# Performance work log

Hardware: AMD Instinct MI355X
Metric: run time of the kernel (lower is better)

Reference implementation:

```python
import jax, jax.numpy as jnp
import numpy as np

B, D_IN, FD = 32768, 2048, 128
N1 = N2 = N3 = 4
T = 1.0  # temperature buffer value (eval mode)
LN_EPS = 1e-5

def _gelu(x):
    return jax.nn.gelu(x, approximate=False)  # torch nn.GELU default = exact erf

def setup_inputs() -> dict:
    key = jax.random.key(0)
    ks = iter(jax.random.split(key, 64))
    def rn(shape, s=0.02):
        return jax.random.normal(next(ks), shape, jnp.float32) * s
    inp = {"x": jax.random.normal(next(ks), (B, D_IN), jnp.float32)}
    # input_proj: Linear(2048,512) GELU Linear(512,256) LayerNorm(256)
    inp.update(ipW1=rn((D_IN, 512)), ipb1=jnp.zeros(512), ipW2=rn((512, 256)), ipb2=jnp.zeros(256),
               ln_g=jnp.ones(256), ln_b=jnp.zeros(256))
    def level(din, nc, pfx):
        return {pfx+"W3d": rn((din, 3)), pfx+"b3d": jnp.zeros(3),
                pfx+"c": rn((nc, 3), 0.3), pfx+"lr": jnp.zeros(nc),
                pfx+"f1W": rn((din, FD)), pfx+"f1b": jnp.zeros(FD),
                pfx+"f2W": rn((FD, FD)), pfx+"f2b": jnp.zeros(FD),
                pfx+"rW": rn((FD+3, nc)), pfx+"rb": jnp.zeros(nc)}
    inp.update(level(256, N1, "l1"))
    inp.update(level(FD, N2, "l2"))
    inp.update(level(FD, N3, "l3"))
    # expert_head: Linear(128+4+4+4, 256) GELU Linear(256, 64)
    inp.update(ehW1=rn((FD+N1+N2+N3, 256)), ehb1=jnp.zeros(256),
               ehW2=rn((256, N1*N2*N3)), ehb2=jnp.zeros(N1*N2*N3))
    return inp

def _level_fwd(x, W3d, b3d, c, f1W, f1b, f2W, f2b, rW, rb):
    # x: (B, din) -> probs (B, nc), features (B, FD)
    pos = x @ W3d + b3d                                   # (B, 3)
    d_sq = ((pos[:, None, :] - c[None, :, :]) ** 2).sum(-1)  # (B, nc)
    geo = -d_sq / (2.0 * T * T + 1e-8)                    # non-spectral geo signal
    feat = _gelu(x @ f1W + f1b) @ f2W + f2b               # (B, FD)
    logits = jnp.concatenate([feat, pos], axis=-1) @ rW + rb + 0.5 * geo
    probs = jax.nn.softmax(logits / max(T, 0.1), axis=-1)  # eval path: plain softmax
    return probs, feat

def _router_fwd(x, ipW1, ipb1, ipW2, ipb2, ln_g, ln_b,
                l1W3d, l1b3d, l1c, l1f1W, l1f1b, l1f2W, l1f2b, l1rW, l1rb,
                l2W3d, l2b3d, l2c, l2f1W, l2f1b, l2f2W, l2f2b, l2rW, l2rb,
                l3W3d, l3b3d, l3c, l3f1W, l3f1b, l3f2W, l3f2b, l3rW, l3rb,
                ehW1, ehb1, ehW2, ehb2):
    h = _gelu(x @ ipW1 + ipb1) @ ipW2 + ipb2
    mu = h.mean(-1, keepdims=True)
    var = ((h - mu) ** 2).mean(-1, keepdims=True)
    h = (h - mu) * jax.lax.rsqrt(var + LN_EPS) * ln_g + ln_b  # LayerNorm(256)
    p1, f1 = _level_fwd(h,  l1W3d, l1b3d, l1c, l1f1W, l1f1b, l1f2W, l1f2b, l1rW, l1rb)
    p2, f2 = _level_fwd(f1, l2W3d, l2b3d, l2c, l2f1W, l2f1b, l2f2W, l2f2b, l2rW, l2rb)
    p3, f3 = _level_fwd(f2, l3W3d, l3b3d, l3c, l3f1W, l3f1b, l3f2W, l3f2b, l3rW, l3rb)
    combined = jnp.concatenate([f3, p1, p2, p3], axis=-1)  # (B, 140)
    logits = _gelu(combined @ ehW1 + ehb1) @ ehW2 + ehb2   # (B, 64)
    expert_probs = jax.nn.softmax(logits / max(T, 0.1), axis=-1)
    return expert_probs

def reference(x, ipW1, ipb1, ipW2, ipb2, ln_g, ln_b,
              l1W3d, l1b3d, l1c, l1lr, l1f1W, l1f1b, l1f2W, l1f2b, l1rW, l1rb,
              l2W3d, l2b3d, l2c, l2lr, l2f1W, l2f1b, l2f2W, l2f2b, l2rW, l2rb,
              l3W3d, l3b3d, l3c, l3lr, l3f1W, l3f1b, l3f2W, l3f2b, l3rW, l3rb,
              ehW1, ehb1, ehW2, ehb2):
    # l?lr (log_radii) are unused in non-spectral mode, matching the source.
    expert_probs = _router_fwd(x, ipW1, ipb1, ipW2, ipb2, ln_g, ln_b,
                               l1W3d, l1b3d, l1c, l1f1W, l1f1b, l1f2W, l1f2b, l1rW, l1rb,
                               l2W3d, l2b3d, l2c, l2f1W, l2f1b, l2f2W, l2f2b, l2rW, l2rb,
                               l3W3d, l3b3d, l3c, l3f1W, l3f1b, l3f2W, l3f2b, l3rW, l3rb,
                               ehW1, ehb1, ehW2, ehb2)
    expert_ids = jnp.argmax(expert_probs, axis=-1)
    return expert_probs, expert_ids
```

## Files before the change

kernel.cpp:

```cpp
#include <hip/hip_runtime.h>
#include <hip/hip_bf16.h>
#include <cstdint>
#include <cstddef>


typedef short  s8v  __attribute__((ext_vector_type(8)));
typedef float  f4v  __attribute__((ext_vector_type(4)));
typedef float  f16v __attribute__((ext_vector_type(16)));
typedef unsigned int u32;

#define B_ROWS 32768

__device__ inline short f2bf(float x) {
    __hip_bfloat16 h = __float2bfloat16(x);
    return __builtin_bit_cast(short, h);
}
__device__ inline float bf2f(short s) {
    return __bfloat162float(__builtin_bit_cast(__hip_bfloat16, s));
}
__device__ inline float gelu_f(float x) {
    return 0.5f * x * (1.0f + erff(x * 0.70710678118654752440f));
}
__device__ inline void gload_lds16(const short* g, short* l) {
    __builtin_amdgcn_global_load_lds(
        (const __attribute__((address_space(1))) u32*)g,
        (__attribute__((address_space(3))) u32*)l, 16, 0, 0);
}

__global__ void split_w1_img(const float* __restrict__ W, short* __restrict__ img)
{
    const int idx = blockIdx.x * 256 + threadIdx.x;
    const int p = idx & 7;
    const int n = (idx >> 3) & 511;
    const int t = idx >> 12;
    const int cs = p ^ (n & 7);
    const int plane = cs >> 2, kc = cs & 3;
    const int kbase = t * 32 + kc * 8;
    s8v v8;
    #pragma unroll
    for (int e = 0; e < 8; ++e) {
        const float v = W[(size_t)(kbase + e) * 512 + n];
        const short h = f2bf(v);
        v8[e] = plane ? f2bf(v - bf2f(h)) : h;
    }
    *(s8v*)&img[(size_t)((t * 512 + n) * 64 + p * 8)] = v8;
}

__launch_bounds__(256, 4)
__global__ void gemm1k(const float* __restrict__ X,
                       const short* __restrict__ Bimg,
                       const float* __restrict__ bias,
                       float* __restrict__ out)
{
    __shared__ short smem[128 * 64 * 2];
    short* Ab = smem;
    short* Bb = smem + 128 * 64;

    const int tid = threadIdx.x;
    const int l = tid & 63, wid = tid >> 6;
    const int wr = wid >> 1, wc = wid & 1;

    const int d = blockIdx.x;
    const int xcd = d & 7, s = d >> 3;
    const int m0 = (xcd * 32 + (s >> 2)) * 128;
    const int n0 = (s & 3) * 128;

    const int ar = tid & 127, ah = tid >> 7;
    const float* xP = X + (size_t)(m0 + ar) * 2048 + ah * 16;
    short* awr = Ab + ar * 64;
    const int pw0 = ((ah * 2    ) ^ (ar & 7)) * 8;
    const int pw1 = ((ah * 2 + 1) ^ (ar & 7)) * 8;
    const int pw2 = ((ah * 2 + 4) ^ (ar & 7)) * 8;
    const int pw3 = ((ah * 2 + 5) ^ (ar & 7)) * 8;

    const short* bP = Bimg + (size_t)n0 * 64 + (size_t)(wid * 4) * 512 + (size_t)l * 8;
    short* bD = Bb + wid * 4 * 512;

    f16v acc[2][2];
    #pragma unroll
    for (int m = 0; m < 2; ++m)
        #pragma unroll
        for (int n = 0; n < 2; ++n) acc[m][n] = (f16v)0.0f;

    f4v cur0, cur1, cur2, cur3;
    cur0 = *(const f4v*)(xP + 0);
    cur1 = *(const f4v*)(xP + 4);
    cur2 = *(const f4v*)(xP + 8);
    cur3 = *(const f4v*)(xP + 12);

    for (int t = 0; t < 64; ++t) {
        s8v hi0, hi1, lo0, lo1;
        #pragma unroll
        for (int e = 0; e < 4; ++e) {
            float v;
            short h;
            v = cur0[e]; h = f2bf(v); hi0[e]     = h; lo0[e]     = f2bf(v - bf2f(h));
            v = cur1[e]; h = f2bf(v); hi0[e + 4] = h; lo0[e + 4] = f2bf(v - bf2f(h));
            v = cur2[e]; h = f2bf(v); hi1[e]     = h; lo1[e]     = f2bf(v - bf2f(h));
            v = cur3[e]; h = f2bf(v); hi1[e + 4] = h; lo1[e + 4] = f2bf(v - bf2f(h));
        }
        __syncthreads();
        *(s8v*)&awr[pw0] = hi0;
        *(s8v*)&awr[pw1] = hi1;
        *(s8v*)&awr[pw2] = lo0;
        *(s8v*)&awr[pw3] = lo1;
        {
            const short* bt = bP + (size_t)t * 32768;
            gload_lds16(bt,          bD);
            gload_lds16(bt +  512,   bD + 512);
            gload_lds16(bt + 1024,   bD + 1024);
            gload_lds16(bt + 1536,   bD + 1536);
        }
        if (t < 63) {
            const float* p = xP + (t + 1) * 32;
            cur0 = *(const f4v*)(p + 0);
            cur1 = *(const f4v*)(p + 4);
            cur2 = *(const f4v*)(p + 8);
            cur3 = *(const f4v*)(p + 12);
        }
        __syncthreads();

        #pragma unroll
        for (int ks = 0; ks < 2; ++ks) {
            const int ph0 = ks * 2 + (l >> 5);
            s8v ahf[2], alf[2], bhf[2], blf[2];
            #pragma unroll
            for (int m = 0; m < 2; ++m) {
                const int row = wr * 64 + m * 32 + (l & 31);
                const int ph = ph0 ^ (row & 7);
                ahf[m] = *(const s8v*)&Ab[row * 64 + ph * 8];
                alf[m] = *(const s8v*)&Ab[row * 64 + (ph ^ 4) * 8];
            }
            #pragma unroll
            for (int n = 0; n < 2; ++n) {
                const int col = wc * 64 + n * 32 + (l & 31);
                const int ph = ph0 ^ (col & 7);
                bhf[n] = *(const s8v*)&Bb[col * 64 + ph * 8];
                blf[n] = *(const s8v*)&Bb[col * 64 + (ph ^ 4) * 8];
            }
            #pragma unroll
            for (int m = 0; m < 2; ++m)
                #pragma unroll
                for (int n = 0; n < 2; ++n) {
                    acc[m][n] = __builtin_amdgcn_mfma_f32_32x32x16_bf16(ahf[m], bhf[n], acc[m][n], 0, 0, 0);
                    acc[m][n] = __builtin_amdgcn_mfma_f32_32x32x16_bf16(ahf[m], blf[n], acc[m][n], 0, 0, 0);
                    acc[m][n] = __builtin_amdgcn_mfma_f32_32x32x16_bf16(alf[m], bhf[n], acc[m][n], 0, 0, 0);
                }
        }
    }

    #pragma unroll
    for (int m = 0; m < 2; ++m) {
        #pragma unroll
        for (int n = 0; n < 2; ++n) {
            const int gcol = n0 + wc * 64 + n * 32 + (l & 31);
            const float bv = bias[gcol];
            #pragma unroll
            for (int r = 0; r < 16; ++r) {
                const int grow = m0 + wr * 64 + m * 32
                               + (r & 3) + 8 * (r >> 2) + 4 * (l >> 5);
                out[(size_t)grow * 512 + gcol] = gelu_f(acc[m][n][r] + bv);
            }
        }
    }
}

struct SplitDesc { const float* W; short* dst; int K, N, Kpad, blk0; };
struct SplitPack { SplitDesc d[9]; };

__global__ void split_all(SplitPack p) {
    const int bid = blockIdx.x;
    int i = 0;
    #pragma unroll
    for (int j = 1; j < 9; ++j) if (bid >= p.d[j].blk0) i = j;
    const SplitDesc& D = p.d[i];
    const int idx = (bid - D.blk0) * 256 + threadIdx.x;
    const int total = D.N * D.Kpad;
    if (idx >= total) return;
    const int n = idx / D.Kpad, k = idx - n * D.Kpad;
    const float v = (k < D.K) ? D.W[(size_t)k * D.N + n] : 0.0f;
    const short hs = f2bf(v);
    D.dst[idx] = hs;
    D.dst[total + idx] = f2bf(v - bf2f(hs));
}

template<int BM, int BN, int EPI>
__launch_bounds__(256, 2)
__global__ void gemm32(const float* __restrict__ A, int lda,
                       const short* __restrict__ Bsp, int ldb, int NK,
                       const float* __restrict__ bias, int K, int N, int ntiles,
                       int ostr, float* __restrict__ out, float* __restrict__ out2)
{
    constexpr int MF  = BM / 64;
    constexpr int NFw = BN / 64;
    constexpr int BUF = (BM + BN) * 64;
    constexpr int FPT = BM / 8;
    constexpr int TPR = 32 / FPT;
    constexpr int nBI = BN / 32;
    __shared__ short smem[2 * BUF];

    const int tid = threadIdx.x;
    const int l   = tid & 63, wid = tid >> 6;
    const int wr  = wid >> 1, wc = wid & 1;
    const int bid = blockIdx.x;
    const int ntb = bid % ntiles, mtb = bid / ntiles;
    const int m0  = mtb * BM, n0 = ntb * BN;

    const int ar = tid / TPR, aseg = tid % TPR;
    const float* aP = A + (size_t)(m0 + ar) * lda + aseg * FPT;

    const short* bg[nBI];
    {
        const int cs = (l & 7) ^ (l >> 3);
        const int plane = cs >> 2, kslot = cs & 3;
        #pragma unroll
        for (int j = 0; j < nBI; ++j) {
            const int col = (wid * nBI + j) * 8 + (l >> 3);
            bg[j] = Bsp + (size_t)plane * NK + (size_t)(n0 + col) * ldb + kslot * 8;
        }
    }

    f16v acc[MF][NFw];
    #pragma unroll
    for (int m = 0; m < MF; ++m)
        #pragma unroll
        for (int n = 0; n < NFw; ++n) acc[m][n] = (f16v)0.0f;

    f4v areg[FPT / 4];

    auto loadA = [&](int t) {
        const float* p = aP + t * 32;
        #pragma unroll
        for (int i = 0; i < FPT / 4; ++i) areg[i] = *(const f4v*)(p + i * 4);
    };
    auto stageB = [&](int t, short* buf) {
        short* Bb = buf + BM * 64;
        #pragma unroll
        for (int j = 0; j < nBI; ++j)
            gload_lds16(bg[j] + t * 32, Bb + (wid * nBI + j) * 512);
    };
    auto writeA = [&](short* buf) {
        #pragma unroll
        for (int c = 0; c < FPT / 8; ++c) {
            s8v hi, lo;
            #pragma unroll
            for (int e = 0; e < 8; ++e) {
                const float v = areg[c * 2 + (e >> 2)][e & 3];
                const short hs = f2bf(v);
                hi[e] = hs; lo[e] = f2bf(v - bf2f(hs));
            }
            const int csh = aseg * (FPT / 8) + c;
            *(s8v*)&buf[ar * 64 + ((csh    ) ^ (ar & 7)) * 8] = hi;
            *(s8v*)&buf[ar * 64 + ((csh + 4) ^ (ar & 7)) * 8] = lo;
        }
    };
    auto compute = [&](const short* buf) {
        const short* Ab = buf;
        const short* Bb = buf + BM * 64;
        #pragma unroll
        for (int ks = 0; ks < 2; ++ks) {
            const int csb = ks * 2 + (l >> 5);
            s8v ah[MF], al[MF], bh[NFw], bl[NFw];
            #pragma unroll
            for (int m = 0; m < MF; ++m) {
                const int row = wr * (BM / 2) + m * 32 + (l & 31);
                ah[m] = *(const s8v*)&Ab[row * 64 + ((csb    ) ^ (row & 7)) * 8];
                al[m] = *(const s8v*)&Ab[row * 64 + ((csb + 4) ^ (row & 7)) * 8];
            }
            #pragma unroll
            for (int n = 0; n < NFw; ++n) {
                const int col = wc * (BN / 2) + n * 32 + (l & 31);
                bh[n] = *(const s8v*)&Bb[col * 64 + ((csb    ) ^ (col & 7)) * 8];
                bl[n] = *(const s8v*)&Bb[col * 64 + ((csb + 4) ^ (col & 7)) * 8];
            }
            __builtin_amdgcn_s_setprio(1);
            #pragma unroll
            for (int m = 0; m < MF; ++m)
                #pragma unroll
                for (int n = 0; n < NFw; ++n) {
                    acc[m][n] = __builtin_amdgcn_mfma_f32_32x32x16_bf16(ah[m], bh[n], acc[m][n], 0, 0, 0);
                    acc[m][n] = __builtin_amdgcn_mfma_f32_32x32x16_bf16(ah[m], bl[n], acc[m][n], 0, 0, 0);
                    acc[m][n] = __builtin_amdgcn_mfma_f32_32x32x16_bf16(al[m], bh[n], acc[m][n], 0, 0, 0);
                }
            __builtin_amdgcn_s_setprio(0);
        }
    };

    const int NT = K / 32;
    loadA(0);
    stageB(0, smem);
    writeA(smem);
    __syncthreads();
    for (int t = 0; t < NT; ++t) {
        short* curb = smem + (t & 1) * BUF;
        short* nxtb = smem + ((t & 1) ^ 1) * BUF;
        const bool pf = (t + 1 < NT);
        if (pf) { loadA(t + 1); stageB(t + 1, nxtb); }
        compute(curb);
        if (pf) writeA(nxtb);
        __syncthreads();
    }

    if constexpr (EPI <= 1) {
        #pragma unroll
        for (int m = 0; m < MF; ++m) {
            #pragma unroll
            for (int n = 0; n < NFw; ++n) {
                const int gcol = n0 + wc * (BN / 2) + n * 32 + (l & 31);
                const float bv = bias[gcol];
                #pragma unroll
                for (int r = 0; r < 16; ++r) {
                    const int grow = m0 + wr * (BM / 2) + m * 32
                                   + (r & 3) + 8 * (r >> 2) + 4 * (l >> 5);
                    float xv = acc[m][n][r] + bv;
                    if constexpr (EPI == 0) xv = gelu_f(xv);
                    out[(size_t)grow * ostr + gcol] = xv;
                }
            }
        }
    } else {
        float* LT = reinterpret_cast<float*>(smem);
        const int gcolL = wc * 32 + (l & 31);
        const float bv = bias[gcolL];
        #pragma unroll
        for (int r = 0; r < 16; ++r) {
            const int row = wr * 32 + (r & 3) + 8 * (r >> 2) + 4 * (l >> 5);
            LT[row * 64 + gcolL] = acc[0][0][r] + bv;
        }
        __syncthreads();
        const int r = tid >> 2, q = tid & 3;
        const float* Lr = LT + r * 64 + q * 16;
        float mx = Lr[0];
        #pragma unroll
        for (int c = 1; c < 16; ++c) mx = fmaxf(mx, Lr[c]);
        mx = fmaxf(mx, __shfl_xor(mx, 1));
        mx = fmaxf(mx, __shfl_xor(mx, 2));
        float ev[16]; float s = 0.0f;
        #pragma unroll
        for (int c = 0; c < 16; ++c) { ev[c] = expf(Lr[c] - mx); s += ev[c]; }
        s += __shfl_xor(s, 1);
        s += __shfl_xor(s, 2);
        float pmax = -1.0f; int arg = 0;
        #pragma unroll
        for (int c = 0; c < 16; ++c) {
            const float pv = ev[c] / s;
            out[(size_t)(m0 + r) * 64 + q * 16 + c] = pv;
            if (pv > pmax) { pmax = pv; arg = q * 16 + c; }
        }
        #pragma unroll
        for (int off = 1; off <= 2; off <<= 1) {
            const float po = __shfl_xor(pmax, off);
            const int   ao = __shfl_xor(arg, off);
            if (po > pmax || (po == pmax && ao < arg)) { pmax = po; arg = ao; }
        }
        if (q == 0) out2[m0 + r] = (float)arg;
    }
}

__global__ __launch_bounds__(256) void ln_kernel(float* __restrict__ H,
                                                 const float* __restrict__ G,
                                                 const float* __restrict__ Bv)
{
    const int row = blockIdx.x * 4 + (threadIdx.x >> 6);
    const int l   = threadIdx.x & 63;
    float* hr = H + (size_t)row * 256;
    f4v v = *reinterpret_cast<const f4v*>(&hr[l * 4]);
    float s = v[0] + v[1] + v[2] + v[3];
    #pragma unroll
    for (int o = 32; o; o >>= 1) s += __shfl_xor(s, o);
    const float mu = s * 0.00390625f;
    f4v d = v - mu;
    float q = d[0]*d[0] + d[1]*d[1] + d[2]*d[2] + d[3]*d[3];
    #pragma unroll
    for (int o = 32; o; o >>= 1) q += __shfl_xor(q, o);
    const float var = q * 0.00390625f;
    const float sc  = 1.0f / sqrtf(var + 1e-5f);
    f4v gg = *reinterpret_cast<const f4v*>(&G[l * 4]);
    f4v bb = *reinterpret_cast<const f4v*>(&Bv[l * 4]);
    f4v o4 = d * sc * gg + bb;
    *reinterpret_cast<f4v*>(&hr[l * 4]) = o4;
}

__device__ void p_head(int row, int l,
                       const float* __restrict__ X, int din,
                       const float* __restrict__ F, int fstr,
                       const float* __restrict__ W3d, const float* __restrict__ b3d,
                       const float* __restrict__ cc,
                       const float* __restrict__ rW, const float* __restrict__ rb,
                       float* __restrict__ dst)
{
    float px0 = 0.f, px1 = 0.f, px2 = 0.f;
    const int per = din >> 6;
    const float* xr = X + (size_t)row * din;
    for (int i = 0; i < per; ++i) {
        const int k = l + (i << 6);
        const float xv = xr[k];
        px0 += xv * W3d[k*3 + 0];
        px1 += xv * W3d[k*3 + 1];
        px2 += xv * W3d[k*3 + 2];
    }
    float g0 = 0.f, g1 = 0.f, g2 = 0.f, g3 = 0.f;
    const float* fr = F + (size_t)row * fstr;
    #pragma unroll
    for (int i = 0; i < 2; ++i) {
        const int k = l + (i << 6);
        const float fv = fr[k];
        g0 += fv * rW[k*4 + 0]; g1 += fv * rW[k*4 + 1];
        g2 += fv * rW[k*4 + 2]; g3 += fv * rW[k*4 + 3];
    }
    #pragma unroll
    for (int o = 32; o; o >>= 1) {
        px0 += __shfl_xor(px0, o); px1 += __shfl_xor(px1, o); px2 += __shfl_xor(px2, o);
        g0  += __shfl_xor(g0, o);  g1  += __shfl_xor(g1, o);
        g2  += __shfl_xor(g2, o);  g3  += __shfl_xor(g3, o);
    }
    if (l == 0) {
        const float pos0 = px0 + b3d[0], pos1 = px1 + b3d[1], pos2 = px2 + b3d[2];
        float lg[4];
        float mx = -1e30f;
        float gg[4] = {g0, g1, g2, g3};
        #pragma unroll
        for (int c = 0; c < 4; ++c) {
            float a = gg[c] + rb[c]
                    + pos0 * rW[512 + c] + pos1 * rW[516 + c] + pos2 * rW[520 + c];
            const float d0 = pos0 - cc[c*3 + 0];
            const float d1 = pos1 - cc[c*3 + 1];
            const float d2 = pos2 - cc[c*3 + 2];
            a += 0.5f * (-(d0*d0 + d1*d1 + d2*d2) / 2.00000001f);
            lg[c] = a;
            mx = fmaxf(mx, a);
        }
        const float e0 = expf(lg[0]-mx), e1 = expf(lg[1]-mx),
                    e2 = expf(lg[2]-mx), e3 = expf(lg[3]-mx);
        const float s = e0 + e1 + e2 + e3;
        dst[0] = e0/s; dst[1] = e1/s; dst[2] = e2/s; dst[3] = e3/s;
    }
}

struct PAllArgs {
    const float* h2; const float* f1; const float* f2; float* comb;
    const float* W3d[3]; const float* b3d[3]; const float* cc[3];
    const float* rW[3];  const float* rb[3];
};

__global__ __launch_bounds__(256) void p_all(PAllArgs A)
{
    const int row = blockIdx.x * 4 + (threadIdx.x >> 6);
    const int l   = threadIdx.x & 63;
    float* cr = A.comb + (size_t)row * 160;
    p_head(row, l, A.h2, 256, A.f1,  128, A.W3d[0], A.b3d[0], A.cc[0], A.rW[0], A.rb[0], cr + 128);
    p_head(row, l, A.f1, 128, A.f2,  128, A.W3d[1], A.b3d[1], A.cc[1], A.rW[1], A.rb[1], cr + 132);
    p_head(row, l, A.f2, 128, A.comb, 160, A.W3d[2], A.b3d[2], A.cc[2], A.rW[2], A.rb[2], cr + 136);
}

extern "C" void kernel_launch(void* const* d_in, const int* in_sizes, int n_in,
                              void* d_out, int out_size, void* d_ws, size_t ws_size,
                              hipStream_t stream)
{
    (void)in_sizes; (void)n_in; (void)out_size; (void)ws_size;

    const float* x    = (const float*)d_in[0];
    const float* ipW1 = (const float*)d_in[1];
    const float* ipb1 = (const float*)d_in[2];
    const float* ipW2 = (const float*)d_in[3];
    const float* ipb2 = (const float*)d_in[4];
    const float* ln_g = (const float*)d_in[5];
    const float* ln_b = (const float*)d_in[6];
    const float* W3d[3] = {(const float*)d_in[7],  (const float*)d_in[17], (const float*)d_in[27]};
    const float* b3d[3] = {(const float*)d_in[8],  (const float*)d_in[18], (const float*)d_in[28]};
    const float* cc[3]  = {(const float*)d_in[9],  (const float*)d_in[19], (const float*)d_in[29]};
    const float* f1W[3] = {(const float*)d_in[11], (const float*)d_in[21], (const float*)d_in[31]};
    const float* f1b[3] = {(const float*)d_in[12], (const float*)d_in[22], (const float*)d_in[32]};
    const float* f2W[3] = {(const float*)d_in[13], (const float*)d_in[23], (const float*)d_in[33]};
    const float* f2b[3] = {(const float*)d_in[14], (const float*)d_in[24], (const float*)d_in[34]};
    const float* rW[3]  = {(const float*)d_in[15], (const float*)d_in[25], (const float*)d_in[35]};
    const float* rb[3]  = {(const float*)d_in[16], (const float*)d_in[26], (const float*)d_in[36]};
    const float* ehW1 = (const float*)d_in[37];
    const float* ehb1 = (const float*)d_in[38];
    const float* ehW2 = (const float*)d_in[39];
    const float* ehb2 = (const float*)d_in[40];

    size_t off = 0;
    auto take = [&](size_t bytes) -> void* {
        void* p = (char*)d_ws + off;
        off += (bytes + 255) & ~(size_t)255;
        return p;
    };
    auto takeW = [&](int N, int Kpad) -> short* {
        return (short*)take((size_t)2 * N * Kpad * 2);
    };
    short* W1img = (short*)take((size_t)64 * 512 * 64 * 2);
    short* W2s = takeW(256, 512);
    short* L1a = takeW(128, 256);
    short* L1b = takeW(128, 128);
    short* L2a = takeW(128, 128);
    short* L2b = takeW(128, 128);
    short* L3a = takeW(128, 128);
    short* L3b = takeW(128, 128);
    short* E1s = takeW(256, 160);
    short* E2s = takeW(64, 256);
    float* h1  = (float*)take((size_t)B_ROWS * 512 * 4);
    float* h2  = (float*)take((size_t)B_ROWS * 256 * 4);
    float* zg  = (float*)take((size_t)B_ROWS * 128 * 4);
    float* f1  = (float*)take((size_t)B_ROWS * 128 * 4);
    float* f2  = (float*)take((size_t)B_ROWS * 128 * 4);
    float* geh = (float*)take((size_t)B_ROWS * 256 * 4);
    float* comb = h1;

    split_w1_img<<<(64 * 512 * 8) / 256, 256, 0, stream>>>(ipW1, W1img);
    SplitPack sp;
    int blk = 0;
    auto desc = [&](int i, const float* W, short* dst, int K, int N, int Kpad) {
        sp.d[i] = {W, dst, K, N, Kpad, blk};
        blk += (N * Kpad + 255) / 256;
    };
    desc(0, ipW2,   W2s,  512, 256,  512);
    desc(1, f1W[0], L1a,  256, 128,  256);
    desc(2, f2W[0], L1b,  128, 128,  128);
    desc(3, f1W[1], L2a,  128, 128,  128);
    desc(4, f2W[1], L2b,  128, 128,  128);
    desc(5, f1W[2], L3a,  128, 128,  128);
    desc(6, f2W[2], L3b,  128, 128,  128);
    desc(7, ehW1,   E1s,  140, 256,  160);
    desc(8, ehW2,   E2s,  256,  64,  256);
    split_all<<<blk, 256, 0, stream>>>(sp);

    const dim3 blkT(256);
    constexpr int MG128 = B_ROWS / 128;
    constexpr int MG64  = B_ROWS / 64;

    gemm1k<<<1024, blkT, 0, stream>>>(x, W1img, ipb1, h1);
    gemm32<128,128,1><<<MG128*2, blkT, 0, stream>>>(h1, 512, W2s, 512, 256*512, ipb2,
                                                    512, 256, 2, 256, h2, nullptr);
    ln_kernel<<<B_ROWS/4, 256, 0, stream>>>(h2, ln_g, ln_b);

    gemm32<64,128,0><<<MG64, blkT, 0, stream>>>(h2, 256, L1a, 256, 128*256, f1b[0], 256, 128, 1, 128, zg, nullptr);
    gemm32<64,128,1><<<MG64, blkT, 0, stream>>>(zg, 128, L1b, 128, 128*128, f2b[0], 128, 128, 1, 128, f1, nullptr);
    gemm32<64,128,0><<<MG64, blkT, 0, stream>>>(f1, 128, L2a, 128, 128*128, f1b[1], 128, 128, 1, 128, zg, nullptr);
    gemm32<64,128,1><<<MG64, blkT, 0, stream>>>(zg, 128, L2b, 128, 128*128, f2b[1], 128, 128, 1, 128, f2, nullptr);
    gemm32<64,128,0><<<MG64, blkT, 0, stream>>>(f2, 128, L3a, 128, 128*128, f1b[2], 128, 128, 1, 128, zg, nullptr);
    gemm32<64,128,1><<<MG64, blkT, 0, stream>>>(zg, 128, L3b, 128, 128*128, f2b[2], 128, 128, 1, 160, comb, nullptr);

    PAllArgs pa;
    pa.h2 = h2; pa.f1 = f1; pa.f2 = f2; pa.comb = comb;
    for (int i = 0; i < 3; ++i) {
        pa.W3d[i] = W3d[i]; pa.b3d[i] = b3d[i]; pa.cc[i] = cc[i];
        pa.rW[i] = rW[i];   pa.rb[i] = rb[i];
    }
    p_all<<<B_ROWS/4, 256, 0, stream>>>(pa);

    gemm32<64,128,0><<<MG64*2, blkT, 0, stream>>>(comb, 160, E1s, 160, 256*160, ehb1,
                                                  160, 256, 2, 256, geh, nullptr);
    gemm32<64,64,2><<<MG64, blkT, 0, stream>>>(geh, 256, E2s, 256, 64*256, ehb2,
                                               256, 64, 1, 64, (float*)d_out,
                                               (float*)d_out + (size_t)B_ROWS * 64);
}
```

Before: 462.2 us.

## Double-buffer B tile in LDS and prefetch next stage during MFMA compute

Splits the B operand LDS area into two buffers that alternate between steps. The next B tile is issued with global_load_lds, and the next A registers are loaded, before the current tile's MFMAs run, so the loads overlap compute. The two __syncthreads per step become raw s_barrier calls with sched_barrier fences, and MFMA sections run at raised wave priority. LDS use grows by half and launch bounds drop from 4 to 3 waves per SIMD, which lowers occupancy. The code relies on in-order vmcnt behaviour to make the async B loads visible before use.

After: 460.2 us. No clear change (-0.4%).

```diff
diff --git a/kernel.cpp b/kernel.cpp
--- a/kernel.cpp
+++ b/kernel.cpp
@@ -46,15 +46,16 @@
     *(s8v*)&img[(size_t)((t * 512 + n) * 64 + p * 8)] = v8;
 }
 
-__launch_bounds__(256, 4)
+__launch_bounds__(256, 3)
 __global__ void gemm1k(const float* __restrict__ X,
                        const short* __restrict__ Bimg,
                        const float* __restrict__ bias,
                        float* __restrict__ out)
 {
-    __shared__ short smem[128 * 64 * 2];
-    short* Ab = smem;
-    short* Bb = smem + 128 * 64;
+    __shared__ short smem[128 * 64 * 3];
+    short* Ab  = smem;
+    short* Bb0 = smem + 128 * 64;
+    short* Bb1 = smem + 128 * 64 * 2;
 
     const int tid = threadIdx.x;
     const int l = tid & 63, wid = tid >> 6;
@@ -74,7 +75,7 @@
     const int pw3 = ((ah * 2 + 5) ^ (ar & 7)) * 8;
 
     const short* bP = Bimg + (size_t)n0 * 64 + (size_t)(wid * 4) * 512 + (size_t)l * 8;
-    short* bD = Bb + wid * 4 * 512;
+    const int bdo = wid * 4 * 512;
 
     f16v acc[2][2];
     #pragma unroll
@@ -83,43 +84,23 @@
         for (int n = 0; n < 2; ++n) acc[m][n] = (f16v)0.0f;
 
     f4v cur0, cur1, cur2, cur3;
-    cur0 = *(const f4v*)(xP + 0);
-    cur1 = *(const f4v*)(xP + 4);
-    cur2 = *(const f4v*)(xP + 8);
-    cur3 = *(const f4v*)(xP + 12);
-
-    for (int t = 0; t < 64; ++t) {
-        s8v hi0, hi1, lo0, lo1;
-        #pragma unroll
-        for (int e = 0; e < 4; ++e) {
-            float v;
-            short h;
-            v = cur0[e]; h = f2bf(v); hi0[e]     = h; lo0[e]     = f2bf(v - bf2f(h));
-            v = cur1[e]; h = f2bf(v); hi0[e + 4] = h; lo0[e + 4] = f2bf(v - bf2f(h));
-            v = cur2[e]; h = f2bf(v); hi1[e]     = h; lo1[e]     = f2bf(v - bf2f(h));
-            v = cur3[e]; h = f2bf(v); hi1[e + 4] = h; lo1[e + 4] = f2bf(v - bf2f(h));
-        }
-        __syncthreads();
-        *(s8v*)&awr[pw0] = hi0;
-        *(s8v*)&awr[pw1] = hi1;
-        *(s8v*)&awr[pw2] = lo0;
-        *(s8v*)&awr[pw3] = lo1;
-        {
-            const short* bt = bP + (size_t)t * 32768;
-            gload_lds16(bt,          bD);
-            gload_lds16(bt +  512,   bD + 512);
-            gload_lds16(bt + 1024,   bD + 1024);
-            gload_lds16(bt + 1536,   bD + 1536);
-        }
-        if (t < 63) {
-            const float* p = xP + (t + 1) * 32;
-            cur0 = *(const f4v*)(p + 0);
-            cur1 = *(const f4v*)(p + 4);
-            cur2 = *(const f4v*)(p + 8);
-            cur3 = *(const f4v*)(p + 12);
-        }
-        __syncthreads();
-
+
+    auto stageB = [&](int t, short* base) {
+        const short* bt = bP + (size_t)t * 32768;
+        short* bD = base + bdo;
+        gload_lds16(bt,        bD);
+        gload_lds16(bt +  512, bD + 512);
+        gload_lds16(bt + 1024, bD + 1024);
+        gload_lds16(bt + 1536, bD + 1536);
+    };
+    auto loadA = [&](int t) {
+        const float* p = xP + t * 32;
+        cur0 = *(const f4v*)(p + 0);
+        cur1 = *(const f4v*)(p + 4);
+        cur2 = *(const f4v*)(p + 8);
+        cur3 = *(const f4v*)(p + 12);
+    };
+    auto compute = [&](const short* Bb) {
         #pragma unroll
         for (int ks = 0; ks < 2; ++ks) {
             const int ph0 = ks * 2 + (l >> 5);
@@ -138,6 +119,7 @@
                 bhf[n] = *(const s8v*)&Bb[col * 64 + ph * 8];
                 blf[n] = *(const s8v*)&Bb[col * 64 + (ph ^ 4) * 8];
             }
+            __builtin_amdgcn_s_setprio(1);
             #pragma unroll
             for (int m = 0; m < 2; ++m)
                 #pragma unroll
@@ -146,7 +128,42 @@
                     acc[m][n] = __builtin_amdgcn_mfma_f32_32x32x16_bf16(ahf[m], blf[n], acc[m][n], 0, 0, 0);
                     acc[m][n] = __builtin_amdgcn_mfma_f32_32x32x16_bf16(alf[m], bhf[n], acc[m][n], 0, 0, 0);
                 }
-        }
+            __builtin_amdgcn_s_setprio(0);
+        }
+    };
+    auto step = [&](int t, short* bcur, short* bnext) {
+        s8v hi0, hi1, lo0, lo1;
+        #pragma unroll
+        for (int e = 0; e < 4; ++e) {
+            float v; short h;
+            v = cur0[e]; h = f2bf(v); hi0[e]     = h; lo0[e]     = f2bf(v - bf2f(h));
+            v = cur1[e]; h = f2bf(v); hi0[e + 4] = h; lo0[e + 4] = f2bf(v - bf2f(h));
+            v = cur2[e]; h = f2bf(v); hi1[e]     = h; lo1[e]     = f2bf(v - bf2f(h));
+            v = cur3[e]; h = f2bf(v); hi1[e + 4] = h; lo1[e + 4] = f2bf(v - bf2f(h));
+        }
+        __builtin_amdgcn_s_barrier();
+        __builtin_amdgcn_sched_barrier(0);
+        *(s8v*)&awr[pw0] = hi0;
+        *(s8v*)&awr[pw1] = hi1;
+        *(s8v*)&awr[pw2] = lo0;
+        *(s8v*)&awr[pw3] = lo1;
+        if (t < 63) {
+            stageB(t + 1, bnext);
+            __builtin_amdgcn_sched_barrier(0);
+            loadA(t + 1);
+        }
+        asm volatile("s_waitcnt lgkmcnt(0)" ::: "memory");
+        __builtin_amdgcn_s_barrier();
+        __builtin_amdgcn_sched_barrier(0);
+        compute(bcur);
+    };
+
+    stageB(0, Bb0);
+    __builtin_amdgcn_sched_barrier(0);
+    loadA(0);
+    for (int t = 0; t < 64; t += 2) {
+        step(t,     Bb0, Bb1);
+        step(t + 1, Bb1, Bb0);
     }
 
     #pragma unroll
```
